# Kernel tuning notes

Hardware: AMD Instinct MI355X
Metric: run time of the kernel (lower is better)

Reference implementation:

```python
import jax, jax.numpy as jnp
import numpy as np

NSLICES = 4
HID = 512
IN_FEAT = 342   # input_shape - 1 (last column is phase)
OUT = 311
BATCH = 256


def cubic(y0, y1, y2, y3, mu):
    # Catmull-Rom cubic interpolation, as in the original PFNN code
    return (
        (-0.5 * y0 + 1.5 * y1 - 1.5 * y2 + 0.5 * y3) * mu * mu * mu
        + (y0 - 2.5 * y1 + 2.0 * y2 - 0.5 * y3) * mu * mu
        + (-0.5 * y0 + 0.5 * y2) * mu
        + y1
    )


def setup_inputs() -> dict:
    key = jax.random.key(0)
    ks = jax.random.split(key, 7)
    x = jax.random.uniform(ks[0], (BATCH, IN_FEAT + 1), dtype=jnp.float32)
    s = 0.02
    W0 = jax.random.normal(ks[1], (NSLICES, HID, IN_FEAT), dtype=jnp.float32) * s
    b0 = jax.random.normal(ks[2], (NSLICES, HID), dtype=jnp.float32) * s
    W1 = jax.random.normal(ks[3], (NSLICES, HID, HID), dtype=jnp.float32) * s
    b1 = jax.random.normal(ks[4], (NSLICES, HID), dtype=jnp.float32) * s
    W2 = jax.random.normal(ks[5], (NSLICES, OUT, HID), dtype=jnp.float32) * s
    b2 = jax.random.normal(ks[6], (NSLICES, OUT), dtype=jnp.float32) * s
    return {"x": x, "W0": W0, "b0": b0, "W1": W1, "b1": b1, "W2": W2, "b2": b2}


def reference(x, W0, b0, W1, b1, W2, b2):
    phase = x[:, -1]                       # [B]
    pscale = NSLICES * phase
    mu = jnp.mod(pscale, 1.0)              # [B]
    i1 = jnp.floor(pscale).astype(jnp.int32) % NSLICES
    i0 = (i1 - 1) % NSLICES
    i2 = (i1 + 1) % NSLICES
    i3 = (i1 + 2) % NSLICES
    muW = mu[:, None, None]                # broadcast over (out, in)
    mub = mu[:, None]

    Wb0 = cubic(W0[i0], W0[i1], W0[i2], W0[i3], muW)   # [B, 512, 342]
    bb0 = cubic(b0[i0], b0[i1], b0[i2], b0[i3], mub)   # [B, 512]
    Wb1 = cubic(W1[i0], W1[i1], W1[i2], W1[i3], muW)   # [B, 512, 512]
    bb1 = cubic(b1[i0], b1[i1], b1[i2], b1[i3], mub)
    Wb2 = cubic(W2[i0], W2[i1], W2[i2], W2[i3], muW)   # [B, 311, 512]
    bb2 = cubic(b2[i0], b2[i1], b2[i2], b2[i3], mub)

    h = x[:, :-1]                                       # [B, 342]
    h = jax.nn.elu(jnp.einsum('boi,bi->bo', Wb0, h) + bb0)
    h = jax.nn.elu(jnp.einsum('boi,bi->bo', Wb1, h) + bb1)
    out = jnp.einsum('boi,bi->bo', Wb2, h) + bb2        # [B, 311]
    return out
```

## Files before the change

kernel.cpp:

```cpp
#include <hip/hip_runtime.h>
#include <math.h>

#define HID 512
#define IN_FEAT 342
#define OUTD 311
#define BATCH 256
#define KP0 352
#define XROW (IN_FEAT + 1)

#define NT1 32
#define NCC1 16
#define NT2 20
#define NCC2 16
#define NCC0 11

typedef unsigned short u16;
typedef short bf16x8 __attribute__((ext_vector_type(8)));
typedef float f32x4 __attribute__((ext_vector_type(4)));

__device__ __forceinline__ u16 f2bf_rne(float v) {
    unsigned int x = __float_as_uint(v);
    unsigned int r = (x + 0x7fffu + ((x >> 16) & 1u)) >> 16;
    return (u16)r;
}
__device__ __forceinline__ float bf2f(u16 u) {
    return __uint_as_float(((unsigned int)u) << 16);
}

union U8 { u16 u[8]; uint4 v; };

__device__ __forceinline__ void split8(const float* __restrict__ src, bf16x8& hi, bf16x8& lo) {
#pragma unroll
    for (int j = 0; j < 8; j++) {
        u16 h = f2bf_rne(src[j]);
        hi[j] = (short)h;
        lo[j] = (short)f2bf_rne(src[j] - bf2f(h));
    }
}

#define NB0 32
#define KLDS0 360
__global__ __launch_bounds__(512, 1) void layer0_fused(
    const float* __restrict__ W0, const float* __restrict__ W1, const float* __restrict__ W2,
    const float* __restrict__ x, const float* __restrict__ bias,
    u16* __restrict__ F1, u16* __restrict__ F2,
    u16* __restrict__ Ohi, u16* __restrict__ Olo)
{
    __shared__ u16 wlds[4 * NCC0 * 1024];
    __shared__ u16 hlds[2 * NB0 * KLDS0];
    __shared__ float accs[4][NB0][17];

    const int blk = (int)blockIdx.x;
    const int bx = (blk >> 3) & 7;
    const int by = (blk & 7) | ((blk >> 6) << 3);
    const int tid = (int)threadIdx.x;
    const int b0 = bx * NB0;
    const int o0 = by * 16;

    for (int idx = tid; idx < 4 * 16 * 44; idx += 512) {
        int s = idx / (16 * 44);
        int rem = idx - s * (16 * 44);
        int rr = rem / 44, c = rem - rr * 44;
        int k = c * 8;
        const float* rp = W0 + (size_t)(s * 512 + o0 + rr) * IN_FEAT;
        float src[8];
        if (k + 8 <= IN_FEAT) {
            const float2* p2 = reinterpret_cast<const float2*>(rp + k);
            float2 v0 = p2[0], v1 = p2[1], v2 = p2[2], v3 = p2[3];
            src[0] = v0.x; src[1] = v0.y; src[2] = v1.x; src[3] = v1.y;
            src[4] = v2.x; src[5] = v2.y; src[6] = v3.x; src[7] = v3.y;
        } else {
#pragma unroll
            for (int j = 0; j < 8; j++) src[j] = (k + j < IN_FEAT) ? rp[k + j] : 0.f;
        }
        U8 hi, lo;
#pragma unroll
        for (int j = 0; j < 8; j++) {
            u16 h = f2bf_rne(src[j]);
            hi.u[j] = h;
            lo.u[j] = f2bf_rne(src[j] - bf2f(h));
        }
        int cc = c >> 2, lane = (c & 3) * 16 + rr;
        *reinterpret_cast<uint4*>(&wlds[(s * NCC0 + cc) * 1024 + lane * 8])       = hi.v;
        *reinterpret_cast<uint4*>(&wlds[(s * NCC0 + cc) * 1024 + 512 + lane * 8]) = lo.v;
    }

    for (int idx = tid; idx < NB0 * 44; idx += 512) {
        int r = idx / 44, c = idx - r * 44;
        int k = c * 8;
        const float* xr = x + (size_t)(b0 + r) * XROW;
        float src[8];
#pragma unroll
        for (int j = 0; j < 8; j++) {
            int kk = k + j;
            src[j] = (kk < IN_FEAT) ? xr[kk] : 0.f;
        }
        bf16x8 hi, lo;
        split8(src, hi, lo);
        *reinterpret_cast<bf16x8*>(&hlds[r * KLDS0 + k])                 = hi;
        *reinterpret_cast<bf16x8*>(&hlds[NB0 * KLDS0 + r * KLDS0 + k])   = lo;
    }
    __syncthreads();

    const int lane = tid & 63;
    const int w = tid >> 6;
    const int s = w & 3;
    const int t = w >> 2;
    const int m = lane & 15;
    const int q = lane >> 4;

    const u16* wf  = &wlds[s * NCC0 * 1024 + lane * 8];
    const u16* hp  = &hlds[(t * 16 + m) * KLDS0 + q * 8];
    const u16* hpl = &hlds[NB0 * KLDS0 + (t * 16 + m) * KLDS0 + q * 8];

    const int brow = b0 + t * 16 + m;
    const float ps = 4.f * x[(size_t)brow * XROW + IN_FEAT];
    const float fl = floorf(ps);
    const float mu = ps - fl;
    const int i1 = ((int)fl) & 3;
    const int jj = (s - i1) & 3;
    const float mu2 = mu * mu, mu3 = mu2 * mu;
    const float ds = (jj == 0) ? ( 1.5f * mu3 - 2.5f * mu2 + 1.0f)
                   : (jj == 1) ? (-1.5f * mu3 + 2.0f * mu2 + 0.5f * mu)
                   : (jj == 2) ? ( 0.5f * mu3 - 0.5f * mu2)
                   :             (-0.5f * mu3 + mu2 - 0.5f * mu);

    f32x4 a0 = {0.f, 0.f, 0.f, 0.f};
    f32x4 a1 = {0.f, 0.f, 0.f, 0.f};
    f32x4 a2 = {0.f, 0.f, 0.f, 0.f};
#pragma unroll
    for (int cc = 0; cc < NCC0; ++cc) {
        bf16x8 ah = *reinterpret_cast<const bf16x8*>(wf + cc * 1024);
        bf16x8 al = *reinterpret_cast<const bf16x8*>(wf + cc * 1024 + 512);
        bf16x8 bh = *reinterpret_cast<const bf16x8*>(hp + cc * 32);
        bf16x8 bl = *reinterpret_cast<const bf16x8*>(hpl + cc * 32);
        a0 = __builtin_amdgcn_mfma_f32_16x16x32_bf16(ah, bh, a0, 0, 0, 0);
        a1 = __builtin_amdgcn_mfma_f32_16x16x32_bf16(ah, bl, a1, 0, 0, 0);
        a2 = __builtin_amdgcn_mfma_f32_16x16x32_bf16(al, bh, a2, 0, 0, 0);
    }
    __syncthreads();

    f32x4 sum = a0 + a1 + a2;
#pragma unroll
    for (int r = 0; r < 4; ++r) {
        int o = o0 + q * 4 + r;
        accs[s][t * 16 + m][q * 4 + r] = ds * (sum[r] + bias[(size_t)s * HID + o]);
    }
    __syncthreads();

    const int b_l = tid >> 4;
    const int o_l = tid & 15;
    float vv = accs[0][b_l][o_l] + accs[1][b_l][o_l]
             + accs[2][b_l][o_l] + accs[3][b_l][o_l];
    {
        float e = (vv > 0.f) ? vv : expm1f(vv);
        u16 h = f2bf_rne(e);
        const int o = o0 + o_l;
        const int b = b0 + b_l;
        Ohi[(size_t)b * HID + o] = h;
        Olo[(size_t)b * HID + o] = f2bf_rne(e - bf2f(h));
    }

    if (blk < 208) {
        const bool w2j = (blk >= 128);
        int l = w2j ? (blk - 128) : blk;
        int js, jot;
        if (w2j) { js = l / 20; jot = l - js * 20; }
        else     { js = l >> 5; jot = l & 31; }
        u16* Fd = w2j ? (F2 + (size_t)(js * NT2 + jot) * NCC2 * 1024)
                      : (F1 + (size_t)(js * NT1 + jot) * NCC1 * 1024);
        for (int idx = tid; idx < 16 * 64; idx += 512) {
            int rr = idx >> 6, c = idx & 63;
            float src[8] = {0.f, 0.f, 0.f, 0.f, 0.f, 0.f, 0.f, 0.f};
            if (!w2j) {
                const float4* p4 = reinterpret_cast<const float4*>(
                    W1 + (size_t)(js * 512 + jot * 16 + rr) * 512 + c * 8);
                float4 v0 = p4[0], v1 = p4[1];
                src[0] = v0.x; src[1] = v0.y; src[2] = v0.z; src[3] = v0.w;
                src[4] = v1.x; src[5] = v1.y; src[6] = v1.z; src[7] = v1.w;
            } else {
                int orow = jot * 16 + rr;
                if (orow < OUTD) {
                    const float4* p4 = reinterpret_cast<const float4*>(
                        W2 + ((size_t)js * OUTD + orow) * 512 + c * 8);
                    float4 v0 = p4[0], v1 = p4[1];
                    src[0] = v0.x; src[1] = v0.y; src[2] = v0.z; src[3] = v0.w;
                    src[4] = v1.x; src[5] = v1.y; src[6] = v1.z; src[7] = v1.w;
                }
            }
            U8 hi, lo;
#pragma unroll
            for (int j = 0; j < 8; j++) {
                u16 h = f2bf_rne(src[j]);
                hi.u[j] = h;
                lo.u[j] = f2bf_rne(src[j] - bf2f(h));
            }
            int cc = c >> 2, jl = (c & 3) * 16 + rr;
            *reinterpret_cast<uint4*>(Fd + cc * 1024 + jl * 8)       = hi.v;
            *reinterpret_cast<uint4*>(Fd + cc * 1024 + 512 + jl * 8) = lo.v;
        }
    }
}

#define NB 16
#define NTHR 256
template<int KP, int KLDS, int FINAL, int NT, int NBY>
__global__ __launch_bounds__(NTHR, 4) void layer_frag(
    const u16* __restrict__ Wf, const float* __restrict__ x,
    const u16* __restrict__ Hhi, const u16* __restrict__ Hlo,
    const float* __restrict__ bias, int Mb,
    u16* __restrict__ Ohi, u16* __restrict__ Olo, float* __restrict__ outp)
{
    union SharedU {
        u16 h[2][NB * KLDS];
        float acc[4][NB][17];
    };
    __shared__ SharedU sm;

    const int blk = (int)blockIdx.x;
    const int bx = (blk >> 3) & 15;
    const int by = (blk & 7) | ((blk >> 7) << 3);
    if (by >= NBY) return;

    const int tid = (int)threadIdx.x;
    const int b0 = bx * NB;
    const int o0 = by * 16;

    constexpr int CH = KP / 8;
    for (int idx = tid; idx < NB * CH; idx += NTHR) {
        int r = idx / CH, c = idx - r * CH;
        size_t g = (size_t)(b0 + r) * KP + c * 8;
        *reinterpret_cast<uint4*>(&sm.h[0][r * KLDS + c * 8]) =
            *reinterpret_cast<const uint4*>(Hhi + g);
        *reinterpret_cast<uint4*>(&sm.h[1][r * KLDS + c * 8]) =
            *reinterpret_cast<const uint4*>(Hlo + g);
    }
    __syncthreads();

    const int lane = tid & 63;
    const int s = tid >> 6;
    const int m = lane & 15;
    const int q = lane >> 4;

    constexpr int NCC = KP / 32;
    const u16* wf = Wf + ((size_t)(s * NT + by) * NCC) * 1024 + lane * 8;
    const u16* hp  = &sm.h[0][m * KLDS + q * 8];
    const u16* hpl = &sm.h[1][m * KLDS + q * 8];

    const int brow = b0 + m;
    const float ps = 4.f * x[(size_t)brow * XROW + IN_FEAT];
    const float fl = floorf(ps);
    const float mu = ps - fl;
    const int i1 = ((int)fl) & 3;
    const int jj = (s - i1) & 3;
    const float mu2 = mu * mu, mu3 = mu2 * mu;
    const float ds = (jj == 0) ? ( 1.5f * mu3 - 2.5f * mu2 + 1.0f)
                   : (jj == 1) ? (-1.5f * mu3 + 2.0f * mu2 + 0.5f * mu)
                   : (jj == 2) ? ( 0.5f * mu3 - 0.5f * mu2)
                   :             (-0.5f * mu3 + mu2 - 0.5f * mu);

    f32x4 a0 = {0.f, 0.f, 0.f, 0.f};
    f32x4 a1 = {0.f, 0.f, 0.f, 0.f};
    f32x4 a2 = {0.f, 0.f, 0.f, 0.f};
#pragma unroll
    for (int cc = 0; cc < NCC; ++cc) {
        bf16x8 ah = *reinterpret_cast<const bf16x8*>(wf + cc * 1024);
        bf16x8 al = *reinterpret_cast<const bf16x8*>(wf + cc * 1024 + 512);
        bf16x8 bh = *reinterpret_cast<const bf16x8*>(hp + cc * 32);
        bf16x8 bl = *reinterpret_cast<const bf16x8*>(hpl + cc * 32);
        a0 = __builtin_amdgcn_mfma_f32_16x16x32_bf16(ah, bh, a0, 0, 0, 0);
        a1 = __builtin_amdgcn_mfma_f32_16x16x32_bf16(ah, bl, a1, 0, 0, 0);
        a2 = __builtin_amdgcn_mfma_f32_16x16x32_bf16(al, bh, a2, 0, 0, 0);
    }
    __syncthreads();

    f32x4 sum = a0 + a1 + a2;
#pragma unroll
    for (int r = 0; r < 4; ++r) {
        int o = o0 + q * 4 + r;
        float bb = (o < Mb) ? bias[(size_t)s * Mb + o] : 0.f;
        sm.acc[s][m][q * 4 + r] = ds * (sum[r] + bb);
    }
    __syncthreads();

    const int b_l = tid >> 4;
    const int o_l = tid & 15;
    float vv = sm.acc[0][b_l][o_l] + sm.acc[1][b_l][o_l]
             + sm.acc[2][b_l][o_l] + sm.acc[3][b_l][o_l];
    const int o = o0 + o_l;
    const int b = b0 + b_l;
    if (!FINAL) {
        float e = (vv > 0.f) ? vv : expm1f(vv);
        u16 h = f2bf_rne(e);
        Ohi[(size_t)b * HID + o] = h;
        Olo[(size_t)b * HID + o] = f2bf_rne(e - bf2f(h));
    } else if (o < OUTD) {
        outp[(size_t)b * OUTD + o] = vv;
    }
}

extern "C" void kernel_launch(void* const* d_in, const int* in_sizes, int n_in,
                              void* d_out, int out_size, void* d_ws, size_t ws_size,
                              hipStream_t stream) {
    const float* x  = (const float*)d_in[0];
    const float* W0 = (const float*)d_in[1];
    const float* b0v = (const float*)d_in[2];
    const float* W1 = (const float*)d_in[3];
    const float* b1v = (const float*)d_in[4];
    const float* W2 = (const float*)d_in[5];
    const float* b2v = (const float*)d_in[6];
    float* out = (float*)d_out;

    char* pw = (char*)d_ws;
    auto alloc = [&](size_t bytes) { char* r = pw; pw += (bytes + 255) & ~(size_t)255; return r; };

    u16* F1 = (u16*)alloc((size_t)4 * NT1 * NCC1 * 1024 * 2);
    u16* F2 = (u16*)alloc((size_t)4 * NT2 * NCC2 * 1024 * 2);
    u16* hahi = (u16*)alloc((size_t)BATCH * HID * 2);
    u16* halo = (u16*)alloc((size_t)BATCH * HID * 2);
    u16* hbhi = (u16*)alloc((size_t)BATCH * HID * 2);
    u16* hblo = (u16*)alloc((size_t)BATCH * HID * 2);

    layer0_fused<<<256, 512, 0, stream>>>(
        W0, W1, W2, x, b0v, F1, F2, hahi, halo);

    layer_frag<HID, 520, 0, NT1, 32><<<512, NTHR, 0, stream>>>(
        F1, x, hahi, halo, b1v, HID, hbhi, hblo, nullptr);

    layer_frag<HID, 520, 1, NT2, 20><<<384, NTHR, 0, stream>>>(
        F2, x, hbhi, hblo, b2v, OUTD, nullptr, nullptr, out);
}
```

Measured before the change: 100.7 us.

## Split-K layers 1 and 2 with atomic accumulation and deferred activation

Layers 1 and 2 now split the 512-wide reduction into two halves, launching twice as many blocks, and accumulate partial results into fp32 buffers with atomic adds. Intermediate activations are stored as fp32 and split into bf16 hi/lo inside the consuming kernel; layer 2's ELU is applied when the next layer loads its input. Otherwise idle blocks of the first kernel zero the accumulation buffers. The aim is more parallelism on a small batch, paid for with atomic traffic, fp32 intermediate bandwidth and non-deterministic summation order.

```diff
diff --git a/kernel.cpp b/kernel.cpp
--- a/kernel.cpp
+++ b/kernel.cpp
@@ -5,7 +5,6 @@
 #define IN_FEAT 342
 #define OUTD 311
 #define BATCH 256
-#define KP0 352
 #define XROW (IN_FEAT + 1)
 
 #define NT1 32
@@ -44,7 +43,7 @@
     const float* __restrict__ W0, const float* __restrict__ W1, const float* __restrict__ W2,
     const float* __restrict__ x, const float* __restrict__ bias,
     u16* __restrict__ F1, u16* __restrict__ F2,
-    u16* __restrict__ Ohi, u16* __restrict__ Olo)
+    float* __restrict__ Oact, float* __restrict__ H2acc, float* __restrict__ outz)
 {
     __shared__ u16 wlds[4 * NCC0 * 1024];
     __shared__ u16 hlds[2 * NB0 * KLDS0];
@@ -97,8 +96,8 @@
         }
         bf16x8 hi, lo;
         split8(src, hi, lo);
-        *reinterpret_cast<bf16x8*>(&hlds[r * KLDS0 + k])                 = hi;
-        *reinterpret_cast<bf16x8*>(&hlds[NB0 * KLDS0 + r * KLDS0 + k])   = lo;
+        *reinterpret_cast<bf16x8*>(&hlds[r * KLDS0 + k])               = hi;
+        *reinterpret_cast<bf16x8*>(&hlds[NB0 * KLDS0 + r * KLDS0 + k]) = lo;
     }
     __syncthreads();
 
@@ -154,11 +153,7 @@
              + accs[2][b_l][o_l] + accs[3][b_l][o_l];
     {
         float e = (vv > 0.f) ? vv : expm1f(vv);
-        u16 h = f2bf_rne(e);
-        const int o = o0 + o_l;
-        const int b = b0 + b_l;
-        Ohi[(size_t)b * HID + o] = h;
-        Olo[(size_t)b * HID + o] = f2bf_rne(e - bf2f(h));
+        Oact[(size_t)(b0 + b_l) * HID + o0 + o_l] = e;
     }
 
     if (blk < 208) {
@@ -199,41 +194,51 @@
             *reinterpret_cast<uint4*>(Fd + cc * 1024 + jl * 8)       = hi.v;
             *reinterpret_cast<uint4*>(Fd + cc * 1024 + 512 + jl * 8) = lo.v;
         }
-    }
-}
-
-#define NB 16
-#define NTHR 256
-template<int KP, int KLDS, int FINAL, int NT, int NBY>
-__global__ __launch_bounds__(NTHR, 4) void layer_frag(
+    } else {
+        for (int i = (blk - 208) * 512 + tid; i < 131072 + 79616; i += 48 * 512) {
+            if (i < 131072) H2acc[i] = 0.f;
+            else            outz[i - 131072] = 0.f;
+        }
+    }
+}
+
+#define KLDS1 264
+template<int FINAL, int ACT, int NT, int NBY>
+__global__ __launch_bounds__(256, 4) void layer_ks(
     const u16* __restrict__ Wf, const float* __restrict__ x,
-    const u16* __restrict__ Hhi, const u16* __restrict__ Hlo,
-    const float* __restrict__ bias, int Mb,
-    u16* __restrict__ Ohi, u16* __restrict__ Olo, float* __restrict__ outp)
+    const float* __restrict__ Hin, const float* __restrict__ bias, int Mb,
+    float* __restrict__ accout)
 {
     union SharedU {
-        u16 h[2][NB * KLDS];
-        float acc[4][NB][17];
+        u16 h[2][16 * KLDS1];
+        float acc[4][16][17];
     };
     __shared__ SharedU sm;
 
     const int blk = (int)blockIdx.x;
     const int bx = (blk >> 3) & 15;
-    const int by = (blk & 7) | ((blk >> 7) << 3);
+    const int kh = (blk >> 7) & 1;
+    const int by = (blk & 7) | ((blk >> 8) << 3);
     if (by >= NBY) return;
 
     const int tid = (int)threadIdx.x;
-    const int b0 = bx * NB;
+    const int b0 = bx * 16;
     const int o0 = by * 16;
 
-    constexpr int CH = KP / 8;
-    for (int idx = tid; idx < NB * CH; idx += NTHR) {
-        int r = idx / CH, c = idx - r * CH;
-        size_t g = (size_t)(b0 + r) * KP + c * 8;
-        *reinterpret_cast<uint4*>(&sm.h[0][r * KLDS + c * 8]) =
-            *reinterpret_cast<const uint4*>(Hhi + g);
-        *reinterpret_cast<uint4*>(&sm.h[1][r * KLDS + c * 8]) =
-            *reinterpret_cast<const uint4*>(Hlo + g);
+    for (int idx = tid; idx < 16 * 32; idx += 256) {
+        int r = idx >> 5, c = idx & 31;
+        const float4* hv = reinterpret_cast<const float4*>(
+            Hin + (size_t)(b0 + r) * HID + kh * 256 + c * 8);
+        float4 v0 = hv[0], v1 = hv[1];
+        float src[8] = {v0.x, v0.y, v0.z, v0.w, v1.x, v1.y, v1.z, v1.w};
+        if (ACT) {
+#pragma unroll
+            for (int j = 0; j < 8; j++) src[j] = (src[j] > 0.f) ? src[j] : expm1f(src[j]);
+        }
+        bf16x8 hi, lo;
+        split8(src, hi, lo);
+        *reinterpret_cast<bf16x8*>(&sm.h[0][r * KLDS1 + c * 8]) = hi;
+        *reinterpret_cast<bf16x8*>(&sm.h[1][r * KLDS1 + c * 8]) = lo;
     }
     __syncthreads();
 
@@ -242,10 +247,9 @@
     const int m = lane & 15;
     const int q = lane >> 4;
 
-    constexpr int NCC = KP / 32;
-    const u16* wf = Wf + ((size_t)(s * NT + by) * NCC) * 1024 + lane * 8;
-    const u16* hp  = &sm.h[0][m * KLDS + q * 8];
-    const u16* hpl = &sm.h[1][m * KLDS + q * 8];
+    const u16* wf = Wf + ((size_t)(s * NT + by) * 16 + kh * 8) * 1024 + lane * 8;
+    const u16* hp  = &sm.h[0][m * KLDS1 + q * 8];
+    const u16* hpl = &sm.h[1][m * KLDS1 + q * 8];
 
     const int brow = b0 + m;
     const float ps = 4.f * x[(size_t)brow * XROW + IN_FEAT];
@@ -263,7 +267,7 @@
     f32x4 a1 = {0.f, 0.f, 0.f, 0.f};
     f32x4 a2 = {0.f, 0.f, 0.f, 0.f};
 #pragma unroll
-    for (int cc = 0; cc < NCC; ++cc) {
+    for (int cc = 0; cc < 8; ++cc) {
         bf16x8 ah = *reinterpret_cast<const bf16x8*>(wf + cc * 1024);
         bf16x8 al = *reinterpret_cast<const bf16x8*>(wf + cc * 1024 + 512);
         bf16x8 bh = *reinterpret_cast<const bf16x8*>(hp + cc * 32);
@@ -278,7 +282,7 @@
 #pragma unroll
     for (int r = 0; r < 4; ++r) {
         int o = o0 + q * 4 + r;
-        float bb = (o < Mb) ? bias[(size_t)s * Mb + o] : 0.f;
+        float bb = (kh == 0 && o < Mb) ? bias[(size_t)s * Mb + o] : 0.f;
         sm.acc[s][m][q * 4 + r] = ds * (sum[r] + bb);
     }
     __syncthreads();
@@ -289,13 +293,10 @@
              + sm.acc[2][b_l][o_l] + sm.acc[3][b_l][o_l];
     const int o = o0 + o_l;
     const int b = b0 + b_l;
-    if (!FINAL) {
-        float e = (vv > 0.f) ? vv : expm1f(vv);
-        u16 h = f2bf_rne(e);
-        Ohi[(size_t)b * HID + o] = h;
-        Olo[(size_t)b * HID + o] = f2bf_rne(e - bf2f(h));
-    } else if (o < OUTD) {
-        outp[(size_t)b * OUTD + o] = vv;
+    if (FINAL) {
+        if (o < OUTD) unsafeAtomicAdd(&accout[(size_t)b * OUTD + o], vv);
+    } else {
+        unsafeAtomicAdd(&accout[(size_t)b * HID + o], vv);
     }
 }
 
@@ -316,17 +317,15 @@
 
     u16* F1 = (u16*)alloc((size_t)4 * NT1 * NCC1 * 1024 * 2);
     u16* F2 = (u16*)alloc((size_t)4 * NT2 * NCC2 * 1024 * 2);
-    u16* hahi = (u16*)alloc((size_t)BATCH * HID * 2);
-    u16* halo = (u16*)alloc((size_t)BATCH * HID * 2);
-    u16* hbhi = (u16*)alloc((size_t)BATCH * HID * 2);
-    u16* hblo = (u16*)alloc((size_t)BATCH * HID * 2);
+    float* H0act = (float*)alloc((size_t)BATCH * HID * 4);
+    float* H2acc = (float*)alloc((size_t)BATCH * HID * 4);
 
     layer0_fused<<<256, 512, 0, stream>>>(
-        W0, W1, W2, x, b0v, F1, F2, hahi, halo);
-
-    layer_frag<HID, 520, 0, NT1, 32><<<512, NTHR, 0, stream>>>(
-        F1, x, hahi, halo, b1v, HID, hbhi, hblo, nullptr);
-
-    layer_frag<HID, 520, 1, NT2, 20><<<384, NTHR, 0, stream>>>(
-        F2, x, hbhi, hblo, b2v, OUTD, nullptr, nullptr, out);
-}
+        W0, W1, W2, x, b0v, F1, F2, H0act, H2acc, out);
+
+    layer_ks<0, 0, NT1, 32><<<1024, 256, 0, stream>>>(
+        F1, x, H0act, b1v, HID, H2acc);
+
+    layer_ks<1, 1, NT2, 20><<<768, 256, 0, stream>>>(
+        F2, x, H2acc, b2v, OUTD, out);
+}
```

Result: no change. 99.99 us (-0.7%).
